# Optimization experiments

Hardware: AMD Instinct MI355X
Metric: run time of the kernel (lower is better)

## Reference

```python
import jax, jax.numpy as jnp
import numpy as np

B, I, H, T = 256, 256, 512, 400


def setup_inputs() -> dict:
    key = jax.random.key(0)
    k1, k2, k3, k4, k5 = jax.random.split(key, 5)
    s = 1.0 / np.sqrt(H)  # PyTorch LSTMCell init scale (values only matter for realism)
    return {
        "x": jax.random.normal(k1, (B, I, T), dtype=jnp.float32),
        "w_ih": jax.random.normal(k2, (4 * H, I), dtype=jnp.float32) * s,
        "w_hh": jax.random.normal(k3, (4 * H, H), dtype=jnp.float32) * s,
        "b_ih": jax.random.normal(k4, (4 * H,), dtype=jnp.float32) * s,
        "b_hh": jax.random.normal(k5, (4 * H,), dtype=jnp.float32) * s,
    }


def reference(x, w_ih, w_hh, b_ih, b_hh):
    # x: [B, I, T] -> time-major [T, B, I]
    x_t = jnp.transpose(x, (2, 0, 1))
    # Precompute input-side gate contributions (batched GEMM, parallel over T)
    xg = jnp.einsum("tbi,gi->tbg", x_t, w_ih) + b_ih + b_hh  # [T, B, 4H]

    h0 = jnp.zeros((x.shape[0], w_hh.shape[1]), dtype=x.dtype)
    c0 = jnp.zeros_like(h0)

    def step(carry, xg_t):
        h, c = carry
        gates = xg_t + h @ w_hh.T  # [B, 4H]
        i, f, g, o = jnp.split(gates, 4, axis=-1)  # PyTorch gate order i,f,g,o
        i = jax.nn.sigmoid(i)
        f = jax.nn.sigmoid(f)
        g = jnp.tanh(g)
        o = jax.nn.sigmoid(o)
        c_new = f * c + i * g
        h_new = o * jnp.tanh(c_new)
        return (h_new, c_new), c_new

    (h_T, c_T), c_stack = jax.lax.scan(step, (h0, c0), xg)
    return c_stack  # [T, B, H] -- the per-step cell states the module stores
```

## Files before the change

kernel.cpp:

```cpp
#include <hip/hip_runtime.h>
#include <stdint.h>

#define TT 400
#define BB 256
#define II 256
#define HH 512
#define NG 2048

typedef __attribute__((ext_vector_type(8))) _Float16 half8;
typedef __attribute__((ext_vector_type(4))) float f32x4;
typedef __attribute__((ext_vector_type(4))) unsigned int u32x4;
typedef unsigned int u32;
typedef unsigned short u16;

static __device__ __forceinline__ u32 f2hbits(float f){
  union { _Float16 h; u16 u; } c; c.h = (_Float16)f; return (u32)c.u;
}

#define GLOAD16(gsrc, ldst) \
  __builtin_amdgcn_global_load_lds((const __attribute__((address_space(1))) void*)(gsrc), \
                                   (__attribute__((address_space(3))) void*)(ldst), 16, 0, 0)

__global__ __launch_bounds__(256) void k_prep_x(const float* __restrict__ x,
                                                u16* __restrict__ xT){
  __shared__ float tile[32][17];
  const int bid = blockIdx.x;
  const int tb = bid % 25, ib = (bid / 25) & 7, b = bid / 200;
  const int t0 = tb * 16, i0 = ib * 32;
  const int tl = threadIdx.x & 15, il = threadIdx.x >> 4;
  tile[il][tl]      = x[(size_t)(b * II + i0 + il) * TT + t0 + tl];
  tile[il + 16][tl] = x[(size_t)(b * II + i0 + il + 16) * TT + t0 + tl];
  __syncthreads();
  const int t_l = threadIdx.x >> 4, ip = threadIdx.x & 15;
  const u32 pack = f2hbits(tile[2 * ip][t_l]) | (f2hbits(tile[2 * ip + 1][t_l]) << 16);
  *(u32*)(xT + ((size_t)(t0 + t_l) * BB + b) * II + i0 + 2 * ip) = pack;
}

__global__ __launch_bounds__(256) void k_prep_w(const float* __restrict__ w_ih,
                                                u16* __restrict__ Wp){
  const size_t idx = (size_t)blockIdx.x * 256 + threadIdx.x;
  const float4 v = *(const float4*)(w_ih + idx * 4);
  uint2 o;
  o.x = f2hbits(v.x) | (f2hbits(v.y) << 16);
  o.y = f2hbits(v.z) | (f2hbits(v.w) << 16);
// ... 53 lines not shown
        const int r = wm + mt * 16 + lr;
        a[mt] = *(const half8*)(lA + r * 128 + ((s ^ (r & 7)) << 4));
      }
      #pragma unroll
      for (int nt = 0; nt < 4; ++nt){
        const int r = wn + nt * 16 + lr;
        b[nt] = *(const half8*)(lB + r * 128 + ((s ^ (r & 7)) << 4));
      }
      #pragma unroll
      for (int mt = 0; mt < 4; ++mt)
        #pragma unroll
        for (int nt = 0; nt < 4; ++nt)
          acc[mt][nt] = __builtin_amdgcn_mfma_f32_16x16x32_f16(a[mt], b[nt], acc[mt][nt], 0, 0, 0);
    }
    __syncthreads();
  }
  #pragma unroll
  for (int mt = 0; mt < 4; ++mt)
    #pragma unroll
    for (int nt = 0; nt < 4; ++nt)
      #pragma unroll
      for (int r = 0; r < 4; ++r){
        const size_t row = m0 + wm + mt * 16 + lh * 4 + r;
        const int col = n0 + wn + nt * 16 + lr;
        xg[row * NG + col] = (_Float16)acc[mt][nt][r];
      }
}

__global__ __launch_bounds__(512) void k_lstm(const _Float16* __restrict__ xg,
    const float* __restrict__ w_hh, const float* __restrict__ b_ih,
    const float* __restrict__ b_hh, u32* __restrict__ htag,
    float* __restrict__ out){
  extern __shared__ char lds[];
  char* Wl = lds;
  char* hb = lds + 131072;
  float* gbuf = (float*)(lds + 147456);

  const int tid = threadIdx.x, w = tid >> 6, lane = tid & 63;
  const int lr = lane & 15, lh = lane >> 4;
  const int gb = blockIdx.x >> 4, gn = blockIdx.x & 15;
  const int b0 = gb * 16, j0 = gn * 32;

  for (int rep = 0; rep < 16; ++rep){
    const int u = rep * 512 + tid;
    const int row = u >> 6, u0 = u & 63;
    const int grow = ((row >> 5) << 9) + j0 + (row & 31);
    const float* src = w_hh + (size_t)grow * HH + u0 * 8;
    const float4 va = *(const float4*)src;
    const float4 vb = *(const float4*)(src + 4);
    union { _Float16 h[8]; u32x4 v; } p;
    p.h[0] = (_Float16)va.x; p.h[1] = (_Float16)va.y;
    p.h[2] = (_Float16)va.z; p.h[3] = (_Float16)va.w;
    p.h[4] = (_Float16)vb.x; p.h[5] = (_Float16)vb.y;
    p.h[6] = (_Float16)vb.z; p.h[7] = (_Float16)vb.w;
    *(u32x4*)(Wl + row * 1024 + ((u0 ^ (row & 7)) << 4)) = p.v;
  }
  const int brow = tid >> 5;
  const int jj   = tid & 31;
  float bias_[4];
  #pragma unroll
  for (int q = 0; q < 4; ++q) bias_[q] = b_ih[q * HH + j0 + jj] + b_hh[q * HH + j0 + jj];
  float c = 0.f;
  const int q = w >> 1, jb = w & 1;

  const int u1 = tid, u2 = tid + 512;
  const int r1 = u1 >> 6, c1 = u1 & 63;
  const int r2 = u2 >> 6, c2 = u2 & 63;
  const size_t gof1 = (size_t)(b0 + r1) * 512 + c1 * 8;
  const size_t gof2 = (size_t)(b0 + r2) * 512 + c2 * 8;
  const int lof1 = r1 * 1024 + ((c1 ^ (r1 & 7)) << 4);
  const int lof2 = r2 * 1024 + ((c2 ^ (r2 & 7)) << 4);
  u32* pst0 = htag + (size_t)(b0 + brow) * 512 + (j0 + jj);
  __syncthreads();

  for (int t = 0; t < TT; ++t){
    const _Float16* xt = xg + (size_t)t * (BB * NG) + (size_t)(b0 + brow) * NG + j0 + jj;
    u32 xv0, xv1, xv2, xv3;
    asm volatile(
      "global_load_ushort %0, %4, off\n\t"
      "global_load_ushort %1, %5, off\n\t"
      "global_load_ushort %2, %6, off\n\t"
      "global_load_ushort %3, %7, off"
      : "=&v"(xv0), "=&v"(xv1), "=&v"(xv2), "=&v"(xv3)
      : "v"(xt), "v"(xt + HH), "v"(xt + 2 * HH), "v"(xt + 3 * HH)
      : "memory");

    if (t > 0){
      const u32* gbase = htag + (size_t)((t - 1) & 1) * 131072;
      const u32* g1 = gbase + gof1;
      const u32* g2 = gbase + gof2;
      const u32 te = ((u32)t) << 16;
      u32x4 a0, a1, d0, d1;
      int need = 3, guard = 0;
      do {
        if (need & 1)
          asm volatile("global_load_dwordx4 %0, %2, off sc0 sc1\n\t"
                       "global_load_dwordx4 %1, %3, off sc0 sc1"
                       : "=&v"(a0), "=&v"(a1) : "v"(g1), "v"(g1 + 4) : "memory");
        if (need & 2)
          asm volatile("global_load_dwordx4 %0, %2, off sc0 sc1\n\t"
                       "global_load_dwordx4 %1, %3, off sc0 sc1"
                       : "=&v"(d0), "=&v"(d1) : "v"(g2), "v"(g2 + 4) : "memory");
        asm volatile("s_waitcnt vmcnt(0)" ::: "memory");
        if (need & 1){
          u32 m = (a0[0]^te)|(a0[1]^te)|(a0[2]^te)|(a0[3]^te)
                 |(a1[0]^te)|(a1[1]^te)|(a1[2]^te)|(a1[3]^te);
          if (!(m >> 16)) need &= ~1;
        }
        if (need & 2){
          u32 m = (d0[0]^te)|(d0[1]^te)|(d0[2]^te)|(d0[3]^te)
                 |(d1[0]^te)|(d1[1]^te)|(d1[2]^te)|(d1[3]^te);
          if (!(m >> 16)) need &= ~2;
        }
      } while (need && ++guard < (1 << 18));
      u32x4 p1, p2;
      p1[0] = (a0[0] & 0xffffu) | (a0[1] << 16);
      p1[1] = (a0[2] & 0xffffu) | (a0[3] << 16);
      p1[2] = (a1[0] & 0xffffu) | (a1[1] << 16);
      p1[3] = (a1[2] & 0xffffu) | (a1[3] << 16);
      p2[0] = (d0[0] & 0xffffu) | (d0[1] << 16);
      p2[1] = (d0[2] & 0xffffu) | (d0[3] << 16);
      p2[2] = (d1[0] & 0xffffu) | (d1[1] << 16);
      p2[3] = (d1[2] & 0xffffu) | (d1[3] << 16);
      *(u32x4*)(hb + lof1) = p1;
      *(u32x4*)(hb + lof2) = p2;
      __syncthreads();
      f32x4 ac0 = {0.f,0.f,0.f,0.f}, ac1 = {0.f,0.f,0.f,0.f};
      const int nrow = q * 32 + jb * 16 + lr;
      const int nbase = nrow * 1024, nx = nrow & 7, ax = lr & 7;
      const char* abase = hb + lr * 1024;
      #pragma unroll
      for (int ks = 0; ks < 16; ks += 2){
        const int s0 = ks * 4 + lh, s1 = s0 + 4;
        const half8 av0 = *(const half8*)(abase + ((s0 ^ ax) << 4));
        const half8 bv0 = *(const half8*)(Wl + nbase + ((s0 ^ nx) << 4));
        ac0 = __builtin_amdgcn_mfma_f32_16x16x32_f16(av0, bv0, ac0, 0, 0, 0);
        const half8 av1 = *(const half8*)(abase + ((s1 ^ ax) << 4));
        const half8 bv1 = *(const half8*)(Wl + nbase + ((s1 ^ nx) << 4));
        ac1 = __builtin_amdgcn_mfma_f32_16x16x32_f16(av1, bv1, ac1, 0, 0, 0);
      }
      const f32x4 acs = ac0 + ac1;
      #pragma unroll
      for (int r = 0; r < 4; ++r)
        gbuf[(q * 16 + lh * 4 + r) * 32 + jb * 16 + lr] = acs[r];
      __syncthreads();
    }
    asm volatile("s_waitcnt vmcnt(0)" ::: "memory");
    asm volatile("" : "+v"(xv0), "+v"(xv1), "+v"(xv2), "+v"(xv3));

    float g4[4];
    {
      union { u32 u; _Float16 h[2]; } cv;
      cv.u = xv0; g4[0] = (float)cv.h[0] + bias_[0];
      cv.u = xv1; g4[1] = (float)cv.h[0] + bias_[1];
      cv.u = xv2; g4[2] = (float)cv.h[0] + bias_[2];
      cv.u = xv3; g4[3] = (float)cv.h[0] + bias_[3];
    }
    if (t > 0){
      #pragma unroll
      for (int qq = 0; qq < 4; ++qq) g4[qq] += gbuf[(qq * 16 + brow) * 32 + jj];
    }
    const float i_ = 1.f / (1.f + __expf(-g4[0]));
    const float f_ = 1.f / (1.f + __expf(-g4[1]));
    const float ea = __expf(-2.f * fabsf(g4[2]));
    const float g_ = __builtin_copysignf((1.f - ea) / (1.f + ea), g4[2]);
    const float o_ = 1.f / (1.f + __expf(-g4[3]));
    c = f_ * c + i_ * g_;
    const float eb = __expf(-2.f * fabsf(c));
    const float th = __builtin_copysignf((1.f - eb) / (1.f + eb), c);
    const float hn = o_ * th;

    if (t < TT - 1){
      u32* ph = pst0 + (size_t)(t & 1) * 131072;
      const u32 hv = f2hbits(hn) | ((u32)(t + 1) << 16);
      asm volatile("global_store_dword %0, %1, off sc0 sc1"
                   :: "v"(ph), "v"(hv) : "memory");
    }
    out[(size_t)t * (BB * HH) + (size_t)(b0 + brow) * HH + j0 + jj] = c;
  }
}

extern "C" void kernel_launch(void* const* d_in, const int* in_sizes, int n_in,
                              void* d_out, int out_size, void* d_ws, size_t ws_size,
                              hipStream_t stream){
  const float* x    = (const float*)d_in[0];
  const float* w_ih = (const float*)d_in[1];
  const float* w_hh = (const float*)d_in[2];
  const float* b_ih = (const float*)d_in[3];
  const float* b_hh = (const float*)d_in[4];
  float* out = (float*)d_out;
  char* ws = (char*)d_ws;

  const size_t o_xg  = 0;
  const size_t o_xt  = 419430400;
  const size_t o_wp  = 471859200;
  const size_t o_h   = 472907776;
  const size_t need  = 473956352;
  if (ws_size < need) return;

  _Float16* xg = (_Float16*)(ws + o_xg);
  u16* xt  = (u16*)(ws + o_xt);
  u16* wp  = (u16*)(ws + o_wp);
  u32* ht  = (u32*)(ws + o_h);

  hipLaunchKernelGGL(k_prep_x, dim3(51200), dim3(256), 0, stream, x, xt);
  hipLaunchKernelGGL(k_prep_w, dim3(512), dim3(256), 0, stream, w_ih, wp);
  hipLaunchKernelGGL(k_gemm_xg, dim3(12800), dim3(256), 0, stream, xt, wp, xg);
  hipLaunchKernelGGL(k_lstm, dim3(256), dim3(512), 155648, stream,
                     xg, w_hh, b_ih, b_hh, ht, out);
}
```

Measured before the change: 1.817 ms.

## Split LSTM block into two batch halves and overlap h exchange with MFMA

Each recurrent block now handles 32 batch rows as two 16-row halves, and the grid is halved to 128 blocks. Loads of the next half's hidden state and input gates are issued speculatively before the current half's MFMA and pointwise work, so cross-block communication latency is hidden behind compute. The h tag buffer is zeroed with a memset to make the speculative tag checks safe. The trade-off is fewer blocks, so half the CUs sit idle, plus more per-block serial work and double-buffered LDS.

```diff
diff --git a/kernel.cpp b/kernel.cpp
--- a/kernel.cpp
+++ b/kernel.cpp
@@ -10,6 +10,7 @@
 typedef __attribute__((ext_vector_type(8))) _Float16 half8;
 typedef __attribute__((ext_vector_type(4))) float f32x4;
 typedef __attribute__((ext_vector_type(4))) unsigned int u32x4;
+typedef __attribute__((ext_vector_type(2))) unsigned int u32x2;
 typedef unsigned int u32;
 typedef unsigned short u16;
 
@@ -129,14 +130,16 @@
     const float* __restrict__ b_hh, u32* __restrict__ htag,
     float* __restrict__ out){
   extern __shared__ char lds[];
-  char* Wl = lds;
-  char* hb = lds + 131072;
-  float* gbuf = (float*)(lds + 147456);
+  char* Wl  = lds;
+  char* hbA = lds + 131072;
+  char* hbB = lds + 147456;
+  float* gbufA = (float*)(lds + 147456);
+  float* gbufB = (float*)(lds + 131072);
 
   const int tid = threadIdx.x, w = tid >> 6, lane = tid & 63;
   const int lr = lane & 15, lh = lane >> 4;
-  const int gb = blockIdx.x >> 4, gn = blockIdx.x & 15;
-  const int b0 = gb * 16, j0 = gn * 32;
+  const int mg = blockIdx.x >> 4, gn = blockIdx.x & 15;
+  const int b0 = mg * 32, j0 = gn * 32;
 
   for (int rep = 0; rep < 16; ++rep){
     const int u = rep * 512 + tid;
@@ -152,129 +155,181 @@
     p.h[6] = (_Float16)vb.z; p.h[7] = (_Float16)vb.w;
     *(u32x4*)(Wl + row * 1024 + ((u0 ^ (row & 7)) << 4)) = p.v;
   }
-  const int brow = tid >> 5;
-  const int jj   = tid & 31;
-  float bias_[4];
+  const int brow = tid >> 5, jj = tid & 31;
+  float biasv[4];
   #pragma unroll
-  for (int q = 0; q < 4; ++q) bias_[q] = b_ih[q * HH + j0 + jj] + b_hh[q * HH + j0 + jj];
-  float c = 0.f;
+  for (int q2 = 0; q2 < 4; ++q2)
+    biasv[q2] = b_ih[q2 * HH + j0 + jj] + b_hh[q2 * HH + j0 + jj];
+  float cA = 0.f, cB = 0.f;
   const int q = w >> 1, jb = w & 1;
-
-  const int u1 = tid, u2 = tid + 512;
-  const int r1 = u1 >> 6, c1 = u1 & 63;
-  const int r2 = u2 >> 6, c2 = u2 & 63;
-  const size_t gof1 = (size_t)(b0 + r1) * 512 + c1 * 8;
-  const size_t gof2 = (size_t)(b0 + r2) * 512 + c2 * 8;
-  const int lof1 = r1 * 1024 + ((c1 ^ (r1 & 7)) << 4);
-  const int lof2 = r2 * 1024 + ((c2 ^ (r2 & 7)) << 4);
-  u32* pst0 = htag + (size_t)(b0 + brow) * 512 + (j0 + jj);
+  const int nrow = q * 32 + jb * 16 + lr;
+  const int nbase = nrow * 1024, nx = nrow & 7, ax = lr & 7;
+
+  size_t sgof[4]; int slof[4];
+  #pragma unroll
+  for (int k = 0; k < 4; ++k){
+    const int u = k * 512 + tid;
+    const int row = u >> 7, cu = u & 127;
+    sgof[k] = (size_t)row * 512 + cu * 4;
+    slof[k] = row * 1024 + ((((cu >> 1) ^ (row & 7)) << 4) | ((cu & 1) << 3));
+  }
+
+#define SPEC_ISSUE(S0,S1,S2,S3, P) \
+  asm volatile("global_load_dwordx4 %0, %4, off sc0 sc1\n\t" \
+               "global_load_dwordx4 %1, %5, off sc0 sc1\n\t" \
+               "global_load_dwordx4 %2, %6, off sc0 sc1\n\t" \
+               "global_load_dwordx4 %3, %7, off sc0 sc1" \
+               : "=&v"(S0), "=&v"(S1), "=&v"(S2), "=&v"(S3) \
+               : "v"((P) + sgof[0]), "v"((P) + sgof[1]), \
+                 "v"((P) + sgof[2]), "v"((P) + sgof[3]) : "memory")
+
+#define XG_ISSUE(X0,X1,X2,X3, PT) \
+  asm volatile("global_load_ushort %0, %4, off\n\t" \
+               "global_load_ushort %1, %5, off\n\t" \
+               "global_load_ushort %2, %6, off\n\t" \
+               "global_load_ushort %3, %7, off" \
+               : "=&v"(X0), "=&v"(X1), "=&v"(X2), "=&v"(X3) \
+               : "v"(PT), "v"((PT) + HH), "v"((PT) + 2 * HH), "v"((PT) + 3 * HH) \
+               : "memory")
+
+#define SPEC_CONSUME(S0,S1,S2,S3, P, TE, HB) do { \
+  asm volatile("" : "+v"(S0), "+v"(S1), "+v"(S2), "+v"(S3)); \
+  int need_ = 15, guard_ = 0; \
+  while (true){ \
+    u32 m_; \
+    if (need_ & 1){ m_ = (S0[0]^(TE))|(S0[1]^(TE))|(S0[2]^(TE))|(S0[3]^(TE)); if (!(m_ >> 16)) need_ &= ~1; } \
+    if (need_ & 2){ m_ = (S1[0]^(TE))|(S1[1]^(TE))|(S1[2]^(TE))|(S1[3]^(TE)); if (!(m_ >> 16)) need_ &= ~2; } \
+    if (need_ & 4){ m_ = (S2[0]^(TE))|(S2[1]^(TE))|(S2[2]^(TE))|(S2[3]^(TE)); if (!(m_ >> 16)) need_ &= ~4; } \
+    if (need_ & 8){ m_ = (S3[0]^(TE))|(S3[1]^(TE))|(S3[2]^(TE))|(S3[3]^(TE)); if (!(m_ >> 16)) need_ &= ~8; } \
+    if (!need_ || ++guard_ >= (1 << 18)) break; \
+    if (need_ & 1) asm volatile("global_load_dwordx4 %0, %1, off sc0 sc1" : "=&v"(S0) : "v"((P) + sgof[0]) : "memory"); \
+    if (need_ & 2) asm volatile("global_load_dwordx4 %0, %1, off sc0 sc1" : "=&v"(S1) : "v"((P) + sgof[1]) : "memory"); \
+    if (need_ & 4) asm volatile("global_load_dwordx4 %0, %1, off sc0 sc1" : "=&v"(S2) : "v"((P) + sgof[2]) : "memory"); \
+    if (need_ & 8) asm volatile("global_load_dwordx4 %0, %1, off sc0 sc1" : "=&v"(S3) : "v"((P) + sgof[3]) : "memory"); \
+    asm volatile("s_waitcnt vmcnt(0)" ::: "memory"); \
+    __builtin_amdgcn_sched_barrier(0); \
+    asm volatile("" : "+v"(S0), "+v"(S1), "+v"(S2), "+v"(S3)); \
+  } \
+  u32x2 w0_, w1_, w2_, w3_; \
+  w0_[0] = (S0[0] & 0xffffu) | (S0[1] << 16); w0_[1] = (S0[2] & 0xffffu) | (S0[3] << 16); \
+  w1_[0] = (S1[0] & 0xffffu) | (S1[1] << 16); w1_[1] = (S1[2] & 0xffffu) | (S1[3] << 16); \
+  w2_[0] = (S2[0] & 0xffffu) | (S2[1] << 16); w2_[1] = (S2[2] & 0xffffu) | (S2[3] << 16); \
+  w3_[0] = (S3[0] & 0xffffu) | (S3[1] << 16); w3_[1] = (S3[2] & 0xffffu) | (S3[3] << 16); \
+  *(u32x2*)((HB) + slof[0]) = w0_; *(u32x2*)((HB) + slof[1]) = w1_; \
+  *(u32x2*)((HB) + slof[2]) = w2_; *(u32x2*)((HB) + slof[3]) = w3_; \
+} while (0)
+
+#define PHASE_ENTRY(T) do { \
+  if ((T) == 0) asm volatile("s_waitcnt vmcnt(0)" ::: "memory"); \
+  else          asm volatile("s_waitcnt vmcnt(2)" ::: "memory"); \
+  __builtin_amdgcn_sched_barrier(0); \
+} while (0)
+
+#define GEMM_PHASE(HB, GB) do { \
+  f32x4 ac0 = {0.f,0.f,0.f,0.f}, ac1 = {0.f,0.f,0.f,0.f}; \
+  const char* abase_ = (HB) + lr * 1024; \
+  _Pragma("unroll") \
+  for (int ks = 0; ks < 16; ks += 2){ \
+    const int s0_ = ks * 4 + lh, s1_ = s0_ + 4; \
+    const half8 av0 = *(const half8*)(abase_ + ((s0_ ^ ax) << 4)); \
+    const half8 bv0 = *(const half8*)(Wl + nbase + ((s0_ ^ nx) << 4)); \
+    ac0 = __builtin_amdgcn_mfma_f32_16x16x32_f16(av0, bv0, ac0, 0, 0, 0); \
+    const half8 av1 = *(const half8*)(abase_ + ((s1_ ^ ax) << 4)); \
+    const half8 bv1 = *(const half8*)(Wl + nbase + ((s1_ ^ nx) << 4)); \
+    ac1 = __builtin_amdgcn_mfma_f32_16x16x32_f16(av1, bv1, ac1, 0, 0, 0); \
+  } \
+  const f32x4 acs_ = ac0 + ac1; \
+  _Pragma("unroll") \
+  for (int r = 0; r < 4; ++r) \
+    (GB)[(q * 16 + lh * 4 + r) * 32 + jb * 16 + lr] = acs_[r]; \
+} while (0)
+
+#define POINTWISE(X0,X1,X2,X3, GB, CREF, ROFF, T) do { \
+  asm volatile("" : "+v"(X0), "+v"(X1), "+v"(X2), "+v"(X3)); \
+  float g4_[4]; \
+  union { u32 u; _Float16 h[2]; } cv_; \
+  cv_.u = X0; g4_[0] = (float)cv_.h[0] + biasv[0]; \
+  cv_.u = X1; g4_[1] = (float)cv_.h[0] + biasv[1]; \
+  cv_.u = X2; g4_[2] = (float)cv_.h[0] + biasv[2]; \
+  cv_.u = X3; g4_[3] = (float)cv_.h[0] + biasv[3]; \
+  if ((T) > 0){ \
+    g4_[0] += (GB)[(0 * 16 + brow) * 32 + jj]; \
+    g4_[1] += (GB)[(1 * 16 + brow) * 32 + jj]; \
+    g4_[2] += (GB)[(2 * 16 + brow) * 32 + jj]; \
+    g4_[3] += (GB)[(3 * 16 + brow) * 32 + jj]; \
+  } \
+  const float i_ = 1.f / (1.f + __expf(-g4_[0])); \
+  const float f_ = 1.f / (1.f + __expf(-g4_[1])); \
+  const float ea_ = __expf(-2.f * fabsf(g4_[2])); \
+  const float g_ = __builtin_copysignf((1.f - ea_) / (1.f + ea_), g4_[2]); \
+  const float o_ = 1.f / (1.f + __expf(-g4_[3])); \
+  CREF = f_ * CREF + i_ * g_; \
+  const float eb_ = __expf(-2.f * fabsf(CREF)); \
+  const float th_ = __builtin_copysignf((1.f - eb_) / (1.f + eb_), CREF); \
+  const float hn_ = o_ * th_; \
+  if ((T) < TT - 1){ \
+    u32* ph_ = htag + (size_t)((T) & 1) * 131072 + (size_t)(b0 + (ROFF) + brow) * 512 + j0 + jj; \
+    const u32 hv_ = f2hbits(hn_) | ((u32)((T) + 1) << 16); \
+    asm volatile("global_store_dword %0, %1, off sc0 sc1" :: "v"(ph_), "v"(hv_) : "memory"); \
+  } \
+  out[(size_t)(T) * (BB * HH) + (size_t)(b0 + (ROFF) + brow) * HH + j0 + jj] = CREF; \
+} while (0)
+
+  u32x4 sA0, sA1, sA2, sA3, sB0, sB1, sB2, sB3;
+  u32 xa0, xa1, xa2, xa3, xb0, xb1, xb2, xb3;
+
+  {
+    const _Float16* pt = xg + (size_t)(b0 + brow) * NG + j0 + jj;
+    XG_ISSUE(xa0, xa1, xa2, xa3, pt);
+  }
   __syncthreads();
 
   for (int t = 0; t < TT; ++t){
-    const _Float16* xt = xg + (size_t)t * (BB * NG) + (size_t)(b0 + brow) * NG + j0 + jj;
-    u32 xv0, xv1, xv2, xv3;
-    asm volatile(
-      "global_load_ushort %0, %4, off\n\t"
-      "global_load_ushort %1, %5, off\n\t"
-      "global_load_ushort %2, %6, off\n\t"
-      "global_load_ushort %3, %7, off"
-      : "=&v"(xv0), "=&v"(xv1), "=&v"(xv2), "=&v"(xv3)
-      : "v"(xt), "v"(xt + HH), "v"(xt + 2 * HH), "v"(xt + 3 * HH)
-      : "memory");
-
+    const u32 te = ((u32)t) << 16;
+    PHASE_ENTRY(t);
     if (t > 0){
-      const u32* gbase = htag + (size_t)((t - 1) & 1) * 131072;
-      const u32* g1 = gbase + gof1;
-      const u32* g2 = gbase + gof2;
-      const u32 te = ((u32)t) << 16;
-      u32x4 a0, a1, d0, d1;
-      int need = 3, guard = 0;
-      do {
-        if (need & 1)
-          asm volatile("global_load_dwordx4 %0, %2, off sc0 sc1\n\t"
-                       "global_load_dwordx4 %1, %3, off sc0 sc1"
-                       : "=&v"(a0), "=&v"(a1) : "v"(g1), "v"(g1 + 4) : "memory");
-        if (need & 2)
-          asm volatile("global_load_dwordx4 %0, %2, off sc0 sc1\n\t"
-                       "global_load_dwordx4 %1, %3, off sc0 sc1"
-                       : "=&v"(d0), "=&v"(d1) : "v"(g2), "v"(g2 + 4) : "memory");
-        asm volatile("s_waitcnt vmcnt(0)" ::: "memory");
-        if (need & 1){
-          u32 m = (a0[0]^te)|(a0[1]^te)|(a0[2]^te)|(a0[3]^te)
-                 |(a1[0]^te)|(a1[1]^te)|(a1[2]^te)|(a1[3]^te);
-          if (!(m >> 16)) need &= ~1;
-        }
-        if (need & 2){
-          u32 m = (d0[0]^te)|(d0[1]^te)|(d0[2]^te)|(d0[3]^te)
-                 |(d1[0]^te)|(d1[1]^te)|(d1[2]^te)|(d1[3]^te);
-          if (!(m >> 16)) need &= ~2;
-        }
-      } while (need && ++guard < (1 << 18));
-      u32x4 p1, p2;
-      p1[0] = (a0[0] & 0xffffu) | (a0[1] << 16);
-      p1[1] = (a0[2] & 0xffffu) | (a0[3] << 16);
-      p1[2] = (a1[0] & 0xffffu) | (a1[1] << 16);
-      p1[3] = (a1[2] & 0xffffu) | (a1[3] << 16);
-      p2[0] = (d0[0] & 0xffffu) | (d0[1] << 16);
-      p2[1] = (d0[2] & 0xffffu) | (d0[3] << 16);
-      p2[2] = (d1[0] & 0xffffu) | (d1[1] << 16);
-      p2[3] = (d1[2] & 0xffffu) | (d1[3] << 16);
-      *(u32x4*)(hb + lof1) = p1;
-      *(u32x4*)(hb + lof2) = p2;
+      u32* pbA = htag + (size_t)((t - 1) & 1) * 131072 + (size_t)b0 * 512;
+      SPEC_CONSUME(sA0, sA1, sA2, sA3, pbA, te, hbA);
       __syncthreads();
-      f32x4 ac0 = {0.f,0.f,0.f,0.f}, ac1 = {0.f,0.f,0.f,0.f};
-      const int nrow = q * 32 + jb * 16 + lr;
-      const int nbase = nrow * 1024, nx = nrow & 7, ax = lr & 7;
-      const char* abase = hb + lr * 1024;
-      #pragma unroll
-      for (int ks = 0; ks < 16; ks += 2){
-        const int s0 = ks * 4 + lh, s1 = s0 + 4;
-        const half8 av0 = *(const half8*)(abase + ((s0 ^ ax) << 4));
-        const half8 bv0 = *(const half8*)(Wl + nbase + ((s0 ^ nx) << 4));
-        ac0 = __builtin_amdgcn_mfma_f32_16x16x32_f16(av0, bv0, ac0, 0, 0, 0);
-        const half8 av1 = *(const half8*)(abase + ((s1 ^ ax) << 4));
-        const half8 bv1 = *(const half8*)(Wl + nbase + ((s1 ^ nx) << 4));
-        ac1 = __builtin_amdgcn_mfma_f32_16x16x32_f16(av1, bv1, ac1, 0, 0, 0);
+      {
+        u32* pbB = htag + (size_t)((t - 1) & 1) * 131072 + (size_t)(b0 + 16) * 512;
+        SPEC_ISSUE(sB0, sB1, sB2, sB3, pbB);
+        const _Float16* pt = xg + (size_t)t * (BB * NG) + (size_t)(b0 + 16 + brow) * NG + j0 + jj;
+        XG_ISSUE(xb0, xb1, xb2, xb3, pt);
       }
-      const f32x4 acs = ac0 + ac1;
-      #pragma unroll
-      for (int r = 0; r < 4; ++r)
-        gbuf[(q * 16 + lh * 4 + r) * 32 + jb * 16 + lr] = acs[r];
+      GEMM_PHASE(hbA, gbufA);
       __syncthreads();
-    }
-    asm volatile("s_waitcnt vmcnt(0)" ::: "memory");
-    asm volatile("" : "+v"(xv0), "+v"(xv1), "+v"(xv2), "+v"(xv3));
-
-    float g4[4];
-    {
-      union { u32 u; _Float16 h[2]; } cv;
-      cv.u = xv0; g4[0] = (float)cv.h[0] + bias_[0];
-      cv.u = xv1; g4[1] = (float)cv.h[0] + bias_[1];
-      cv.u = xv2; g4[2] = (float)cv.h[0] + bias_[2];
-      cv.u = xv3; g4[3] = (float)cv.h[0] + bias_[3];
-    }
+    } else {
+      const _Float16* pt = xg + (size_t)(b0 + 16 + brow) * NG + j0 + jj;
+      XG_ISSUE(xb0, xb1, xb2, xb3, pt);
+    }
+    POINTWISE(xa0, xa1, xa2, xa3, gbufA, cA, 0, t);
+    __syncthreads();
+    PHASE_ENTRY(t);
     if (t > 0){
-      #pragma unroll
-      for (int qq = 0; qq < 4; ++qq) g4[qq] += gbuf[(qq * 16 + brow) * 32 + jj];
-    }
-    const float i_ = 1.f / (1.f + __expf(-g4[0]));
-    const float f_ = 1.f / (1.f + __expf(-g4[1]));
-    const float ea = __expf(-2.f * fabsf(g4[2]));
-    const float g_ = __builtin_copysignf((1.f - ea) / (1.f + ea), g4[2]);
-    const float o_ = 1.f / (1.f + __expf(-g4[3]));
-    c = f_ * c + i_ * g_;
-    const float eb = __expf(-2.f * fabsf(c));
-    const float th = __builtin_copysignf((1.f - eb) / (1.f + eb), c);
-    const float hn = o_ * th;
-
+      u32* pbB = htag + (size_t)((t - 1) & 1) * 131072 + (size_t)(b0 + 16) * 512;
+      SPEC_CONSUME(sB0, sB1, sB2, sB3, pbB, te, hbB);
+      __syncthreads();
+    }
     if (t < TT - 1){
-      u32* ph = pst0 + (size_t)(t & 1) * 131072;
-      const u32 hv = f2hbits(hn) | ((u32)(t + 1) << 16);
-      asm volatile("global_store_dword %0, %1, off sc0 sc1"
-                   :: "v"(ph), "v"(hv) : "memory");
-    }
-    out[(size_t)t * (BB * HH) + (size_t)(b0 + brow) * HH + j0 + jj] = c;
-  }
+      u32* pbA = htag + (size_t)(t & 1) * 131072 + (size_t)b0 * 512;
+      SPEC_ISSUE(sA0, sA1, sA2, sA3, pbA);
+      const _Float16* pt = xg + (size_t)(t + 1) * (BB * NG) + (size_t)(b0 + brow) * NG + j0 + jj;
+      XG_ISSUE(xa0, xa1, xa2, xa3, pt);
+    }
+    if (t > 0){
+      GEMM_PHASE(hbB, gbufB);
+      __syncthreads();
+    }
+    POINTWISE(xb0, xb1, xb2, xb3, gbufB, cB, 16, t);
+    __syncthreads();
+  }
+#undef SPEC_ISSUE
+#undef XG_ISSUE
+#undef SPEC_CONSUME
+#undef PHASE_ENTRY
+#undef GEMM_PHASE
+#undef POINTWISE
 }
 
 extern "C" void kernel_launch(void* const* d_in, const int* in_sizes, int n_in,
@@ -300,9 +355,10 @@
   u16* wp  = (u16*)(ws + o_wp);
   u32* ht  = (u32*)(ws + o_h);
 
+  hipMemsetAsync(ht, 0, 1048576, stream);
   hipLaunchKernelGGL(k_prep_x, dim3(51200), dim3(256), 0, stream, x, xt);
   hipLaunchKernelGGL(k_prep_w, dim3(512), dim3(256), 0, stream, w_ih, wp);
   hipLaunchKernelGGL(k_gemm_xg, dim3(12800), dim3(256), 0, stream, xt, wp, xg);
-  hipLaunchKernelGGL(k_lstm, dim3(256), dim3(512), 155648, stream,
+  hipLaunchKernelGGL(k_lstm, dim3(128), dim3(512), 163840, stream,
                      xg, w_hh, b_ih, b_hh, ht, out);
 }
```

Measured after the change: 1.981 ms. 9.1% more time.

## Restructure LSTM recurrence with per-chunk LDS spin consumption and register gate exchange

Applied to the files above, without the earlier changes.

Reworks the persistent LSTM kernel so each wave polls only its own slice of the previous hidden state from global memory and writes tagged words into LDS. Other waves spin on those LDS tags chunk by chunk and issue MFMAs as soon as each chunk is valid, which replaces the full block barrier between the h gather and the GEMM. The weight layout is reordered so each wave computes all four gates for its columns, and ds_bpermute replaces the gbuf LDS round trip and a second barrier. It also prefetches the next step's xg, remaps blocks, and zeroes the tag buffer with a memset. The risks are heavier LDS spinning, more LDS traffic from the wider 16-byte tag entries, and reliance on relaxed LDS atomics for ordering.

```diff
diff --git a/kernel.cpp b/kernel.cpp
--- a/kernel.cpp
+++ b/kernel.cpp
@@ -131,17 +131,16 @@
   extern __shared__ char lds[];
   char* Wl = lds;
   char* hb = lds + 131072;
-  float* gbuf = (float*)(lds + 147456);
 
   const int tid = threadIdx.x, w = tid >> 6, lane = tid & 63;
   const int lr = lane & 15, lh = lane >> 4;
-  const int gb = blockIdx.x >> 4, gn = blockIdx.x & 15;
-  const int b0 = gb * 16, j0 = gn * 32;
+  const int g = blockIdx.x & 15, n = blockIdx.x >> 4;
+  const int b0 = g * 16, j0 = n * 32;
 
   for (int rep = 0; rep < 16; ++rep){
     const int u = rep * 512 + tid;
     const int row = u >> 6, u0 = u & 63;
-    const int grow = ((row >> 5) << 9) + j0 + (row & 31);
+    const int grow = ((row >> 2) & 3) * 512 + j0 + (row >> 4) * 4 + (row & 3);
     const float* src = w_hh + (size_t)grow * HH + u0 * 8;
     const float4 va = *(const float4*)src;
     const float4 vb = *(const float4*)(src + 4);
@@ -150,29 +149,38 @@
     p.h[2] = (_Float16)va.z; p.h[3] = (_Float16)va.w;
     p.h[4] = (_Float16)vb.x; p.h[5] = (_Float16)vb.y;
     p.h[6] = (_Float16)vb.z; p.h[7] = (_Float16)vb.w;
-    *(u32x4*)(Wl + row * 1024 + ((u0 ^ (row & 7)) << 4)) = p.v;
-  }
-  const int brow = tid >> 5;
-  const int jj   = tid & 31;
-  float bias_[4];
+    *(u32x4*)(Wl + row * 1024 + ((u0 ^ (row & 15)) << 4)) = p.v;
+  }
+  {
+    u32x4 z = {0u, 0u, 0u, 0u};
+    #pragma unroll
+    for (int k2 = 0; k2 < 4; ++k2)
+      *(u32x4*)(hb + (k2 * 512 + tid) * 16) = z;
+  }
+
+  const int mcell = lane >> 2, cc = lane & 3;
+  const int col = j0 + w * 4 + cc;
+  const int sel = mcell & 3;
+  float biasv[4];
   #pragma unroll
-  for (int q = 0; q < 4; ++q) bias_[q] = b_ih[q * HH + j0 + jj] + b_hh[q * HH + j0 + jj];
+  for (int q2 = 0; q2 < 4; ++q2)
+    biasv[q2] = b_ih[q2 * HH + col] + b_hh[q2 * HH + col];
   float c = 0.f;
-  const int q = w >> 1, jb = w & 1;
-
-  const int u1 = tid, u2 = tid + 512;
-  const int r1 = u1 >> 6, c1 = u1 & 63;
-  const int r2 = u2 >> 6, c2 = u2 & 63;
-  const size_t gof1 = (size_t)(b0 + r1) * 512 + c1 * 8;
-  const size_t gof2 = (size_t)(b0 + r2) * 512 + c2 * 8;
-  const int lof1 = r1 * 1024 + ((c1 ^ (r1 & 7)) << 4);
-  const int lof2 = r2 * 1024 + ((c2 ^ (r2 & 7)) << 4);
-  u32* pst0 = htag + (size_t)(b0 + brow) * 512 + (j0 + jj);
+
+  const int sr = lane >> 2, sc8 = lane & 3;
+  const int s0 = 2 * w, s1 = 2 * w + 1;
+  const int lbase = sr * 2048;
+  const int la0 = lbase + (((s0 * 8 + sc8 * 2    ) ^ sr) << 4);
+  const int la1 = lbase + (((s0 * 8 + sc8 * 2 + 1) ^ sr) << 4);
+  const int lb0 = lbase + (((s1 * 8 + sc8 * 2    ) ^ sr) << 4);
+  const int lb1 = lbase + (((s1 * 8 + sc8 * 2 + 1) ^ sr) << 4);
+  u32* const hb32 = (u32*)hb;
+
   __syncthreads();
 
-  for (int t = 0; t < TT; ++t){
-    const _Float16* xt = xg + (size_t)t * (BB * NG) + (size_t)(b0 + brow) * NG + j0 + jj;
-    u32 xv0, xv1, xv2, xv3;
+  u32 xv0, xv1, xv2, xv3;
+  {
+    const _Float16* xt = xg + (size_t)(b0 + mcell) * NG + col;
     asm volatile(
       "global_load_ushort %0, %4, off\n\t"
       "global_load_ushort %1, %5, off\n\t"
@@ -181,81 +189,111 @@
       : "=&v"(xv0), "=&v"(xv1), "=&v"(xv2), "=&v"(xv3)
       : "v"(xt), "v"(xt + HH), "v"(xt + 2 * HH), "v"(xt + 3 * HH)
       : "memory");
-
+  }
+
+#define LDSPIN_CONSUME(KS, ACC) do { \
+  const int ua_ = (KS) * 8 + lh * 2; \
+  const int i0_ = (lr * 2048 + ((ua_ ^ lr) << 4)) >> 2; \
+  const int i1_ = (lr * 2048 + (((ua_ + 1) ^ lr) << 4)) >> 2; \
+  u32 f0,f1,f2,f3,f4,f5,f6,f7; int gg_ = 0; \
+  while (true){ \
+    f0 = __hip_atomic_load(hb32 + i0_ + 0, __ATOMIC_RELAXED, __HIP_MEMORY_SCOPE_WORKGROUP); \
+    f1 = __hip_atomic_load(hb32 + i0_ + 1, __ATOMIC_RELAXED, __HIP_MEMORY_SCOPE_WORKGROUP); \
+    f2 = __hip_atomic_load(hb32 + i0_ + 2, __ATOMIC_RELAXED, __HIP_MEMORY_SCOPE_WORKGROUP); \
+    f3 = __hip_atomic_load(hb32 + i0_ + 3, __ATOMIC_RELAXED, __HIP_MEMORY_SCOPE_WORKGROUP); \
+    f4 = __hip_atomic_load(hb32 + i1_ + 0, __ATOMIC_RELAXED, __HIP_MEMORY_SCOPE_WORKGROUP); \
+    f5 = __hip_atomic_load(hb32 + i1_ + 1, __ATOMIC_RELAXED, __HIP_MEMORY_SCOPE_WORKGROUP); \
+    f6 = __hip_atomic_load(hb32 + i1_ + 2, __ATOMIC_RELAXED, __HIP_MEMORY_SCOPE_WORKGROUP); \
+    f7 = __hip_atomic_load(hb32 + i1_ + 3, __ATOMIC_RELAXED, __HIP_MEMORY_SCOPE_WORKGROUP); \
+    const u32 m_ = (f0^te)|(f1^te)|(f2^te)|(f3^te)|(f4^te)|(f5^te)|(f6^te)|(f7^te); \
+    if (!(m_ >> 16) || ++gg_ >= (1 << 16)) break; \
+  } \
+  u32x4 pk_; \
+  pk_[0] = (f0 & 0xffffu) | (f1 << 16); \
+  pk_[1] = (f2 & 0xffffu) | (f3 << 16); \
+  pk_[2] = (f4 & 0xffffu) | (f5 << 16); \
+  pk_[3] = (f6 & 0xffffu) | (f7 << 16); \
+  union { u32x4 v; half8 h; } au_; au_.v = pk_; \
+  const int ub_ = (KS) * 4 + lh; \
+  const half8 bf_ = *(const half8*)(Wl + (w * 16 + lr) * 1024 + ((ub_ ^ lr) << 4)); \
+  ACC = __builtin_amdgcn_mfma_f32_16x16x32_f16(au_.h, bf_, ACC, 0, 0, 0); \
+} while (0)
+
+  for (int t = 0; t < TT; ++t){
+    float g4[4];
     if (t > 0){
-      const u32* gbase = htag + (size_t)((t - 1) & 1) * 131072;
-      const u32* g1 = gbase + gof1;
-      const u32* g2 = gbase + gof2;
+      __syncthreads();
       const u32 te = ((u32)t) << 16;
-      u32x4 a0, a1, d0, d1;
-      int need = 3, guard = 0;
-      do {
-        if (need & 1)
-          asm volatile("global_load_dwordx4 %0, %2, off sc0 sc1\n\t"
-                       "global_load_dwordx4 %1, %3, off sc0 sc1"
-                       : "=&v"(a0), "=&v"(a1) : "v"(g1), "v"(g1 + 4) : "memory");
-        if (need & 2)
-          asm volatile("global_load_dwordx4 %0, %2, off sc0 sc1\n\t"
-                       "global_load_dwordx4 %1, %3, off sc0 sc1"
-                       : "=&v"(d0), "=&v"(d1) : "v"(g2), "v"(g2 + 4) : "memory");
-        asm volatile("s_waitcnt vmcnt(0)" ::: "memory");
-        if (need & 1){
-          u32 m = (a0[0]^te)|(a0[1]^te)|(a0[2]^te)|(a0[3]^te)
-                 |(a1[0]^te)|(a1[1]^te)|(a1[2]^te)|(a1[3]^te);
-          if (!(m >> 16)) need &= ~1;
-        }
-        if (need & 2){
-          u32 m = (d0[0]^te)|(d0[1]^te)|(d0[2]^te)|(d0[3]^te)
-                 |(d1[0]^te)|(d1[1]^te)|(d1[2]^te)|(d1[3]^te);
-          if (!(m >> 16)) need &= ~2;
-        }
-      } while (need && ++guard < (1 << 18));
-      u32x4 p1, p2;
-      p1[0] = (a0[0] & 0xffffu) | (a0[1] << 16);
-      p1[1] = (a0[2] & 0xffffu) | (a0[3] << 16);
-      p1[2] = (a1[0] & 0xffffu) | (a1[1] << 16);
-      p1[3] = (a1[2] & 0xffffu) | (a1[3] << 16);
-      p2[0] = (d0[0] & 0xffffu) | (d0[1] << 16);
-      p2[1] = (d0[2] & 0xffffu) | (d0[3] << 16);
-      p2[2] = (d1[0] & 0xffffu) | (d1[1] << 16);
-      p2[3] = (d1[2] & 0xffffu) | (d1[3] << 16);
-      *(u32x4*)(hb + lof1) = p1;
-      *(u32x4*)(hb + lof2) = p2;
-      __syncthreads();
+      {
+        const u32* gb = htag + (size_t)((t - 1) & 1) * 131072 + (size_t)(b0 + sr) * 512;
+        const u32* pa0 = gb + s0 * 32 + sc8 * 8;
+        const u32* pa1 = pa0 + 4;
+        const u32* pb0 = gb + s1 * 32 + sc8 * 8;
+        const u32* pb1 = pb0 + 4;
+        u32x4 va0, va1, vb0, vb1;
+        int pend = 15, guard = 0;
+        do {
+          if (pend & 1) asm volatile("global_load_dwordx4 %0, %1, off sc0 sc1"
+                                     : "=&v"(va0) : "v"(pa0) : "memory");
+          if (pend & 2) asm volatile("global_load_dwordx4 %0, %1, off sc0 sc1"
+                                     : "=&v"(va1) : "v"(pa1) : "memory");
+          if (pend & 4) asm volatile("global_load_dwordx4 %0, %1, off sc0 sc1"
+                                     : "=&v"(vb0) : "v"(pb0) : "memory");
+          if (pend & 8) asm volatile("global_load_dwordx4 %0, %1, off sc0 sc1"
+                                     : "=&v"(vb1) : "v"(pb1) : "memory");
+          asm volatile("s_waitcnt vmcnt(0)" ::: "memory");
+          __builtin_amdgcn_sched_barrier(0);
+          if (pend & 1){
+            const u32 m_ = (va0[0]^te)|(va0[1]^te)|(va0[2]^te)|(va0[3]^te);
+            if (!(m_ >> 16)){ *(u32x4*)(hb + la0) = va0; pend &= ~1; }
+          }
+          if (pend & 2){
+            const u32 m_ = (va1[0]^te)|(va1[1]^te)|(va1[2]^te)|(va1[3]^te);
+            if (!(m_ >> 16)){ *(u32x4*)(hb + la1) = va1; pend &= ~2; }
+          }
+          if (pend & 4){
+            const u32 m_ = (vb0[0]^te)|(vb0[1]^te)|(vb0[2]^te)|(vb0[3]^te);
+            if (!(m_ >> 16)){ *(u32x4*)(hb + lb0) = vb0; pend &= ~4; }
+          }
+          if (pend & 8){
+            const u32 m_ = (vb1[0]^te)|(vb1[1]^te)|(vb1[2]^te)|(vb1[3]^te);
+            if (!(m_ >> 16)){ *(u32x4*)(hb + lb1) = vb1; pend &= ~8; }
+          }
+          asm volatile("" ::: "memory");
+        } while (pend && ++guard < (1 << 14));
+      }
       f32x4 ac0 = {0.f,0.f,0.f,0.f}, ac1 = {0.f,0.f,0.f,0.f};
-      const int nrow = q * 32 + jb * 16 + lr;
-      const int nbase = nrow * 1024, nx = nrow & 7, ax = lr & 7;
-      const char* abase = hb + lr * 1024;
-      #pragma unroll
-      for (int ks = 0; ks < 16; ks += 2){
-        const int s0 = ks * 4 + lh, s1 = s0 + 4;
-        const half8 av0 = *(const half8*)(abase + ((s0 ^ ax) << 4));
-        const half8 bv0 = *(const half8*)(Wl + nbase + ((s0 ^ nx) << 4));
-        ac0 = __builtin_amdgcn_mfma_f32_16x16x32_f16(av0, bv0, ac0, 0, 0, 0);
-        const half8 av1 = *(const half8*)(abase + ((s1 ^ ax) << 4));
-        const half8 bv1 = *(const half8*)(Wl + nbase + ((s1 ^ nx) << 4));
-        ac1 = __builtin_amdgcn_mfma_f32_16x16x32_f16(av1, bv1, ac1, 0, 0, 0);
+      #pragma unroll
+      for (int i = 0; i < 16; i += 2){
+        const int ksA = (2 * w + i) & 15;
+        const int ksB = (2 * w + i + 1) & 15;
+        LDSPIN_CONSUME(ksA, ac0);
+        LDSPIN_CONSUME(ksB, ac1);
       }
       const f32x4 acs = ac0 + ac1;
       #pragma unroll
-      for (int r = 0; r < 4; ++r)
-        gbuf[(q * 16 + lh * 4 + r) * 32 + jb * 16 + lr] = acs[r];
-      __syncthreads();
-    }
+      for (int q2 = 0; q2 < 4; ++q2){
+        const int addr = ((lane & 48) | (q2 << 2) | cc) << 2;
+        const int r0 = __builtin_amdgcn_ds_bpermute(addr, __float_as_int(acs[0]));
+        const int r1 = __builtin_amdgcn_ds_bpermute(addr, __float_as_int(acs[1]));
+        const int r2 = __builtin_amdgcn_ds_bpermute(addr, __float_as_int(acs[2]));
+        const int r3 = __builtin_amdgcn_ds_bpermute(addr, __float_as_int(acs[3]));
+        const int rv = sel == 0 ? r0 : sel == 1 ? r1 : sel == 2 ? r2 : r3;
+        g4[q2] = __int_as_float(rv);
+      }
+    } else {
+      #pragma unroll
+      for (int q2 = 0; q2 < 4; ++q2) g4[q2] = 0.f;
+    }
+
     asm volatile("s_waitcnt vmcnt(0)" ::: "memory");
     asm volatile("" : "+v"(xv0), "+v"(xv1), "+v"(xv2), "+v"(xv3));
-
-    float g4[4];
     {
       union { u32 u; _Float16 h[2]; } cv;
-      cv.u = xv0; g4[0] = (float)cv.h[0] + bias_[0];
-      cv.u = xv1; g4[1] = (float)cv.h[0] + bias_[1];
-      cv.u = xv2; g4[2] = (float)cv.h[0] + bias_[2];
-      cv.u = xv3; g4[3] = (float)cv.h[0] + bias_[3];
-    }
-    if (t > 0){
-      #pragma unroll
-      for (int qq = 0; qq < 4; ++qq) g4[qq] += gbuf[(qq * 16 + brow) * 32 + jj];
+      cv.u = xv0; g4[0] += (float)cv.h[0] + biasv[0];
+      cv.u = xv1; g4[1] += (float)cv.h[0] + biasv[1];
+      cv.u = xv2; g4[2] += (float)cv.h[0] + biasv[2];
+      cv.u = xv3; g4[3] += (float)cv.h[0] + biasv[3];
     }
     const float i_ = 1.f / (1.f + __expf(-g4[0]));
     const float f_ = 1.f / (1.f + __expf(-g4[1]));
@@ -268,13 +306,23 @@
     const float hn = o_ * th;
 
     if (t < TT - 1){
-      u32* ph = pst0 + (size_t)(t & 1) * 131072;
+      u32* ph = htag + (size_t)(t & 1) * 131072 + (size_t)(b0 + mcell) * 512 + col;
       const u32 hv = f2hbits(hn) | ((u32)(t + 1) << 16);
       asm volatile("global_store_dword %0, %1, off sc0 sc1"
                    :: "v"(ph), "v"(hv) : "memory");
-    }
-    out[(size_t)t * (BB * HH) + (size_t)(b0 + brow) * HH + j0 + jj] = c;
-  }
+      const _Float16* xt = xg + (size_t)(t + 1) * (BB * NG) + (size_t)(b0 + mcell) * NG + col;
+      asm volatile(
+        "global_load_ushort %0, %4, off\n\t"
+        "global_load_ushort %1, %5, off\n\t"
+        "global_load_ushort %2, %6, off\n\t"
+        "global_load_ushort %3, %7, off"
+        : "=&v"(xv0), "=&v"(xv1), "=&v"(xv2), "=&v"(xv3)
+        : "v"(xt), "v"(xt + HH), "v"(xt + 2 * HH), "v"(xt + 3 * HH)
+        : "memory");
+    }
+    out[(size_t)t * (BB * HH) + (size_t)(b0 + mcell) * HH + col] = c;
+  }
+#undef LDSPIN_CONSUME
 }
 
 extern "C" void kernel_launch(void* const* d_in, const int* in_sizes, int n_in,
@@ -300,9 +348,10 @@
   u16* wp  = (u16*)(ws + o_wp);
   u32* ht  = (u32*)(ws + o_h);
 
+  hipMemsetAsync(ht, 0, 1048576, stream);
   hipLaunchKernelGGL(k_prep_x, dim3(51200), dim3(256), 0, stream, x, xt);
   hipLaunchKernelGGL(k_prep_w, dim3(512), dim3(256), 0, stream, w_ih, wp);
   hipLaunchKernelGGL(k_gemm_xg, dim3(12800), dim3(256), 0, stream, xt, wp, xg);
-  hipLaunchKernelGGL(k_lstm, dim3(256), dim3(512), 155648, stream,
+  hipLaunchKernelGGL(k_lstm, dim3(256), dim3(512), 163840, stream,
                      xg, w_hh, b_ih, b_hh, ht, out);
 }
```

Measured after the change: 2.944 ms. 62.1% more time.

## Interleave gate rows per wave, drop gbuf barrier, double-buffer h, prefetch next xg

Applied to the files above, without the earlier changes.

Reorders the W_hh rows in LDS so each wave holds all four gates for four hidden columns. Gate values are exchanged within a wave using ds_bpermute instead of a shared gbuf, which removes the second __syncthreads per timestep. It also double-buffers the h tile in LDS, issues all four tagged h loads at once and only reissues the halves that are not yet ready, and prefetches the next step's xg values. It swaps the block-to-tile mapping, widens the swizzle, and zeroes the tag buffer with a memset. The aim is to shorten the serial per-step critical path, at the cost of more permute instructions and extra LDS.

```diff
diff --git a/kernel.cpp b/kernel.cpp
--- a/kernel.cpp
+++ b/kernel.cpp
@@ -129,19 +129,18 @@
     const float* __restrict__ b_hh, u32* __restrict__ htag,
     float* __restrict__ out){
   extern __shared__ char lds[];
-  char* Wl = lds;
-  char* hb = lds + 131072;
-  float* gbuf = (float*)(lds + 147456);
+  char* Wl  = lds;
+  char* hb0 = lds + 131072;
 
   const int tid = threadIdx.x, w = tid >> 6, lane = tid & 63;
   const int lr = lane & 15, lh = lane >> 4;
-  const int gb = blockIdx.x >> 4, gn = blockIdx.x & 15;
-  const int b0 = gb * 16, j0 = gn * 32;
+  const int g = blockIdx.x & 15, n = blockIdx.x >> 4;
+  const int b0 = g * 16, j0 = n * 32;
 
   for (int rep = 0; rep < 16; ++rep){
     const int u = rep * 512 + tid;
     const int row = u >> 6, u0 = u & 63;
-    const int grow = ((row >> 5) << 9) + j0 + (row & 31);
+    const int grow = ((row >> 2) & 3) * 512 + j0 + (row >> 4) * 4 + (row & 3);
     const float* src = w_hh + (size_t)grow * HH + u0 * 8;
     const float4 va = *(const float4*)src;
     const float4 vb = *(const float4*)(src + 4);
@@ -150,29 +149,32 @@
     p.h[2] = (_Float16)va.z; p.h[3] = (_Float16)va.w;
     p.h[4] = (_Float16)vb.x; p.h[5] = (_Float16)vb.y;
     p.h[6] = (_Float16)vb.z; p.h[7] = (_Float16)vb.w;
-    *(u32x4*)(Wl + row * 1024 + ((u0 ^ (row & 7)) << 4)) = p.v;
+    *(u32x4*)(Wl + row * 1024 + ((u0 ^ (row & 15)) << 4)) = p.v;
   }
-  const int brow = tid >> 5;
-  const int jj   = tid & 31;
-  float bias_[4];
+
+  const int mcell = lane >> 2, cc = lane & 3;
+  const int col = j0 + w * 4 + cc;
+  const int sel = mcell & 3;
+  float biasv[4];
   #pragma unroll
-  for (int q = 0; q < 4; ++q) bias_[q] = b_ih[q * HH + j0 + jj] + b_hh[q * HH + j0 + jj];
+  for (int q2 = 0; q2 < 4; ++q2)
+    biasv[q2] = b_ih[q2 * HH + col] + b_hh[q2 * HH + col];
   float c = 0.f;
-  const int q = w >> 1, jb = w & 1;
 
   const int u1 = tid, u2 = tid + 512;
   const int r1 = u1 >> 6, c1 = u1 & 63;
   const int r2 = u2 >> 6, c2 = u2 & 63;
   const size_t gof1 = (size_t)(b0 + r1) * 512 + c1 * 8;
   const size_t gof2 = (size_t)(b0 + r2) * 512 + c2 * 8;
-  const int lof1 = r1 * 1024 + ((c1 ^ (r1 & 7)) << 4);
-  const int lof2 = r2 * 1024 + ((c2 ^ (r2 & 7)) << 4);
-  u32* pst0 = htag + (size_t)(b0 + brow) * 512 + (j0 + jj);
+  const int lof1 = r1 * 1024 + ((c1 ^ r1) << 4);
+  const int lof2 = r2 * 1024 + ((c2 ^ r2) << 4);
+  u32* pst0 = htag + (size_t)(b0 + mcell) * 512 + col;
+
   __syncthreads();
 
-  for (int t = 0; t < TT; ++t){
-    const _Float16* xt = xg + (size_t)t * (BB * NG) + (size_t)(b0 + brow) * NG + j0 + jj;
-    u32 xv0, xv1, xv2, xv3;
+  u32 xv0, xv1, xv2, xv3;
+  {
+    const _Float16* xt = xg + (size_t)(b0 + mcell) * NG + col;
     asm volatile(
       "global_load_ushort %0, %4, off\n\t"
       "global_load_ushort %1, %5, off\n\t"
@@ -181,81 +183,106 @@
       : "=&v"(xv0), "=&v"(xv1), "=&v"(xv2), "=&v"(xv3)
       : "v"(xt), "v"(xt + HH), "v"(xt + 2 * HH), "v"(xt + 3 * HH)
       : "memory");
-
+  }
+
+  for (int t = 0; t < TT; ++t){
+    float g4[4];
     if (t > 0){
-      const u32* gbase = htag + (size_t)((t - 1) & 1) * 131072;
-      const u32* g1 = gbase + gof1;
-      const u32* g2 = gbase + gof2;
+      char* hb = hb0 + ((t & 1) << 14);
       const u32 te = ((u32)t) << 16;
-      u32x4 a0, a1, d0, d1;
-      int need = 3, guard = 0;
-      do {
-        if (need & 1)
-          asm volatile("global_load_dwordx4 %0, %2, off sc0 sc1\n\t"
-                       "global_load_dwordx4 %1, %3, off sc0 sc1"
-                       : "=&v"(a0), "=&v"(a1) : "v"(g1), "v"(g1 + 4) : "memory");
-        if (need & 2)
-          asm volatile("global_load_dwordx4 %0, %2, off sc0 sc1\n\t"
-                       "global_load_dwordx4 %1, %3, off sc0 sc1"
-                       : "=&v"(d0), "=&v"(d1) : "v"(g2), "v"(g2 + 4) : "memory");
-        asm volatile("s_waitcnt vmcnt(0)" ::: "memory");
-        if (need & 1){
-          u32 m = (a0[0]^te)|(a0[1]^te)|(a0[2]^te)|(a0[3]^te)
-                 |(a1[0]^te)|(a1[1]^te)|(a1[2]^te)|(a1[3]^te);
-          if (!(m >> 16)) need &= ~1;
+      {
+        const u32* gbase = htag + (size_t)((t - 1) & 1) * 131072;
+        const u32* g1 = gbase + gof1;
+        const u32* g2 = gbase + gof2;
+        u32x4 a0, a1, d0, d1;
+        asm volatile(
+          "global_load_dwordx4 %0, %4, off sc0 sc1\n\t"
+          "global_load_dwordx4 %1, %5, off sc0 sc1\n\t"
+          "global_load_dwordx4 %2, %6, off sc0 sc1\n\t"
+          "global_load_dwordx4 %3, %7, off sc0 sc1"
+          : "=&v"(a0), "=&v"(a1), "=&v"(d0), "=&v"(d1)
+          : "v"(g1), "v"(g1 + 4), "v"(g2), "v"(g2 + 4) : "memory");
+        int pend = 3, guard = 0;
+        do {
+          asm volatile("s_waitcnt vmcnt(0)" ::: "memory");
+          __builtin_amdgcn_sched_barrier(0);
+          if (pend & 1){
+            const u32 m_ = (a0[0]^te)|(a0[1]^te)|(a0[2]^te)|(a0[3]^te)
+                          |(a1[0]^te)|(a1[1]^te)|(a1[2]^te)|(a1[3]^te);
+            if (!(m_ >> 16)){
+              u32x4 p1;
+              p1[0] = (a0[0] & 0xffffu) | (a0[1] << 16);
+              p1[1] = (a0[2] & 0xffffu) | (a0[3] << 16);
+              p1[2] = (a1[0] & 0xffffu) | (a1[1] << 16);
+              p1[3] = (a1[2] & 0xffffu) | (a1[3] << 16);
+              *(u32x4*)(hb + lof1) = p1;
+              pend &= ~1;
+            } else {
+              asm volatile("global_load_dwordx4 %0, %2, off sc0 sc1\n\t"
+                           "global_load_dwordx4 %1, %3, off sc0 sc1"
+                           : "=&v"(a0), "=&v"(a1) : "v"(g1), "v"(g1 + 4) : "memory");
+            }
+          }
+          if (pend & 2){
+            const u32 m_ = (d0[0]^te)|(d0[1]^te)|(d0[2]^te)|(d0[3]^te)
+                          |(d1[0]^te)|(d1[1]^te)|(d1[2]^te)|(d1[3]^te);
+            if (!(m_ >> 16)){
+              u32x4 p2;
+              p2[0] = (d0[0] & 0xffffu) | (d0[1] << 16);
+              p2[1] = (d0[2] & 0xffffu) | (d0[3] << 16);
+              p2[2] = (d1[0] & 0xffffu) | (d1[1] << 16);
+              p2[3] = (d1[2] & 0xffffu) | (d1[3] << 16);
+              *(u32x4*)(hb + lof2) = p2;
+              pend &= ~2;
+            } else {
+              asm volatile("global_load_dwordx4 %0, %2, off sc0 sc1\n\t"
+                           "global_load_dwordx4 %1, %3, off sc0 sc1"
+                           : "=&v"(d0), "=&v"(d1) : "v"(g2), "v"(g2 + 4) : "memory");
+            }
+          }
+        } while (pend && ++guard < (1 << 16));
+      }
+      __syncthreads();
+      f32x4 ac0 = {0.f,0.f,0.f,0.f}, ac1 = ac0, ac2 = ac0, ac3 = ac0;
+      const char* arow = hb + lr * 1024;
+      const char* brow = Wl + (w * 16 + lr) * 1024;
+      #pragma unroll
+      for (int ks = 0; ks < 16; ks += 4){
+        #pragma unroll
+        for (int j = 0; j < 4; ++j){
+          const int ua = (ks + j) * 4 + lh;
+          const half8 av = *(const half8*)(arow + ((ua ^ lr) << 4));
+          const half8 bv = *(const half8*)(brow + ((ua ^ lr) << 4));
+          if (j == 0) ac0 = __builtin_amdgcn_mfma_f32_16x16x32_f16(av, bv, ac0, 0, 0, 0);
+          if (j == 1) ac1 = __builtin_amdgcn_mfma_f32_16x16x32_f16(av, bv, ac1, 0, 0, 0);
+          if (j == 2) ac2 = __builtin_amdgcn_mfma_f32_16x16x32_f16(av, bv, ac2, 0, 0, 0);
+          if (j == 3) ac3 = __builtin_amdgcn_mfma_f32_16x16x32_f16(av, bv, ac3, 0, 0, 0);
         }
-        if (need & 2){
-          u32 m = (d0[0]^te)|(d0[1]^te)|(d0[2]^te)|(d0[3]^te)
-                 |(d1[0]^te)|(d1[1]^te)|(d1[2]^te)|(d1[3]^te);
-          if (!(m >> 16)) need &= ~2;
-        }
-      } while (need && ++guard < (1 << 18));
-      u32x4 p1, p2;
-      p1[0] = (a0[0] & 0xffffu) | (a0[1] << 16);
-      p1[1] = (a0[2] & 0xffffu) | (a0[3] << 16);
-      p1[2] = (a1[0] & 0xffffu) | (a1[1] << 16);
-      p1[3] = (a1[2] & 0xffffu) | (a1[3] << 16);
-      p2[0] = (d0[0] & 0xffffu) | (d0[1] << 16);
-      p2[1] = (d0[2] & 0xffffu) | (d0[3] << 16);
-      p2[2] = (d1[0] & 0xffffu) | (d1[1] << 16);
-      p2[3] = (d1[2] & 0xffffu) | (d1[3] << 16);
-      *(u32x4*)(hb + lof1) = p1;
-      *(u32x4*)(hb + lof2) = p2;
-      __syncthreads();
-      f32x4 ac0 = {0.f,0.f,0.f,0.f}, ac1 = {0.f,0.f,0.f,0.f};
-      const int nrow = q * 32 + jb * 16 + lr;
-      const int nbase = nrow * 1024, nx = nrow & 7, ax = lr & 7;
-      const char* abase = hb + lr * 1024;
-      #pragma unroll
-      for (int ks = 0; ks < 16; ks += 2){
-        const int s0 = ks * 4 + lh, s1 = s0 + 4;
-        const half8 av0 = *(const half8*)(abase + ((s0 ^ ax) << 4));
-        const half8 bv0 = *(const half8*)(Wl + nbase + ((s0 ^ nx) << 4));
-        ac0 = __builtin_amdgcn_mfma_f32_16x16x32_f16(av0, bv0, ac0, 0, 0, 0);
-        const half8 av1 = *(const half8*)(abase + ((s1 ^ ax) << 4));
-        const half8 bv1 = *(const half8*)(Wl + nbase + ((s1 ^ nx) << 4));
-        ac1 = __builtin_amdgcn_mfma_f32_16x16x32_f16(av1, bv1, ac1, 0, 0, 0);
-      }
-      const f32x4 acs = ac0 + ac1;
-      #pragma unroll
-      for (int r = 0; r < 4; ++r)
-        gbuf[(q * 16 + lh * 4 + r) * 32 + jb * 16 + lr] = acs[r];
-      __syncthreads();
-    }
+      }
+      const f32x4 acs = (ac0 + ac1) + (ac2 + ac3);
+      #pragma unroll
+      for (int q2 = 0; q2 < 4; ++q2){
+        const int addr = ((lane & 48) | (q2 << 2) | cc) << 2;
+        const int r0 = __builtin_amdgcn_ds_bpermute(addr, __float_as_int(acs[0]));
+        const int r1 = __builtin_amdgcn_ds_bpermute(addr, __float_as_int(acs[1]));
+        const int r2 = __builtin_amdgcn_ds_bpermute(addr, __float_as_int(acs[2]));
+        const int r3 = __builtin_amdgcn_ds_bpermute(addr, __float_as_int(acs[3]));
+        const int rv = sel == 0 ? r0 : sel == 1 ? r1 : sel == 2 ? r2 : r3;
+        g4[q2] = __int_as_float(rv);
+      }
+    } else {
+      #pragma unroll
+      for (int q2 = 0; q2 < 4; ++q2) g4[q2] = 0.f;
+    }
+
     asm volatile("s_waitcnt vmcnt(0)" ::: "memory");
     asm volatile("" : "+v"(xv0), "+v"(xv1), "+v"(xv2), "+v"(xv3));
-
-    float g4[4];
     {
       union { u32 u; _Float16 h[2]; } cv;
-      cv.u = xv0; g4[0] = (float)cv.h[0] + bias_[0];
-      cv.u = xv1; g4[1] = (float)cv.h[0] + bias_[1];
-      cv.u = xv2; g4[2] = (float)cv.h[0] + bias_[2];
-      cv.u = xv3; g4[3] = (float)cv.h[0] + bias_[3];
-    }
-    if (t > 0){
-      #pragma unroll
-      for (int qq = 0; qq < 4; ++qq) g4[qq] += gbuf[(qq * 16 + brow) * 32 + jj];
+      cv.u = xv0; g4[0] += (float)cv.h[0] + biasv[0];
+      cv.u = xv1; g4[1] += (float)cv.h[0] + biasv[1];
+      cv.u = xv2; g4[2] += (float)cv.h[0] + biasv[2];
+      cv.u = xv3; g4[3] += (float)cv.h[0] + biasv[3];
     }
     const float i_ = 1.f / (1.f + __expf(-g4[0]));
     const float f_ = 1.f / (1.f + __expf(-g4[1]));
@@ -272,8 +299,17 @@
       const u32 hv = f2hbits(hn) | ((u32)(t + 1) << 16);
       asm volatile("global_store_dword %0, %1, off sc0 sc1"
                    :: "v"(ph), "v"(hv) : "memory");
-    }
-    out[(size_t)t * (BB * HH) + (size_t)(b0 + brow) * HH + j0 + jj] = c;
+      const _Float16* xt = xg + (size_t)(t + 1) * (BB * NG) + (size_t)(b0 + mcell) * NG + col;
+      asm volatile(
+        "global_load_ushort %0, %4, off\n\t"
+        "global_load_ushort %1, %5, off\n\t"
+        "global_load_ushort %2, %6, off\n\t"
+        "global_load_ushort %3, %7, off"
+        : "=&v"(xv0), "=&v"(xv1), "=&v"(xv2), "=&v"(xv3)
+        : "v"(xt), "v"(xt + HH), "v"(xt + 2 * HH), "v"(xt + 3 * HH)
+        : "memory");
+    }
+    out[(size_t)t * (BB * HH) + (size_t)(b0 + mcell) * HH + col] = c;
   }
 }
 
@@ -300,9 +336,10 @@
   u16* wp  = (u16*)(ws + o_wp);
   u32* ht  = (u32*)(ws + o_h);
 
+  hipMemsetAsync(ht, 0, 1048576, stream);
   hipLaunchKernelGGL(k_prep_x, dim3(51200), dim3(256), 0, stream, x, xt);
   hipLaunchKernelGGL(k_prep_w, dim3(512), dim3(256), 0, stream, w_ih, wp);
   hipLaunchKernelGGL(k_gemm_xg, dim3(12800), dim3(256), 0, stream, xt, wp, xg);
-  hipLaunchKernelGGL(k_lstm, dim3(256), dim3(512), 155648, stream,
+  hipLaunchKernelGGL(k_lstm, dim3(256), dim3(512), 163840, stream,
                      xg, w_hh, b_ih, b_hh, ht, out);
 }
```

After: 4.043 ms. 2.23x slower.
